# Optimization experiments

Hardware: AMD Instinct MI355X
Metric: run time of the kernel (lower is better)

## Reference

```python
import jax, jax.numpy as jnp
import numpy as np

N = 50_000      # nodes
E = 500_000     # directed edges
EMB = 500       # emb_dim (fixed by module)
OUT = 119       # decoder out_dim (num atom types)
L = 5           # encoder num_layer
BN_EPS = 1e-5


def setup_inputs() -> dict:
    key = jax.random.key(0)
    ks = jax.random.split(key, 20)
    d = {}
    # int graph inputs
    atom_type = jax.random.randint(ks[0], (N,), 0, 119)
    chirality = jax.random.randint(ks[1], (N,), 0, 3)
    d["x"] = jnp.stack([atom_type, chirality], axis=1)
    d["edge_index"] = jax.random.randint(ks[2], (2, E), 0, N)
    bond_type = jax.random.randint(ks[3], (E,), 0, 4)  # real bonds (4 = self-loop token)
    bond_dir = jax.random.randint(ks[4], (E,), 0, 3)
    d["edge_attr"] = jnp.stack([bond_type, bond_dir], axis=1)
    d["masked_atom_mask"] = jax.random.bernoulli(ks[5], 0.25, (N,))
    # float params
    f = lambda k, s: (jax.random.normal(k, s) * 0.02).astype(jnp.float32)
    d["atom_emb1"] = f(ks[6], (120, EMB))
    d["atom_emb2"] = f(ks[7], (3, EMB))
    d["enc_eemb1"] = f(ks[8], (L, 6, EMB))
    d["enc_eemb2"] = f(ks[9], (L, 3, EMB))
    d["enc_W1"] = f(ks[10], (L, EMB, 2 * EMB))
    d["enc_b1"] = jnp.zeros((L, 2 * EMB), jnp.float32)
    d["enc_W2"] = f(ks[11], (L, 2 * EMB, EMB))
    d["enc_b2"] = jnp.zeros((L, EMB), jnp.float32)
    d["bn_gamma"] = jnp.ones((L, EMB), jnp.float32)
    d["bn_beta"] = jnp.zeros((L, EMB), jnp.float32)
    d["bn_mean"] = jnp.zeros((L, EMB), jnp.float32)
    d["bn_var"] = jnp.ones((L, EMB), jnp.float32)
    d["prelu_a"] = jnp.float32(0.25)
    d["n2d_W"] = f(ks[12], (EMB, EMB))  # Linear(500,500,bias=False)
    d["dec_eemb1"] = f(ks[13], (6, EMB))
    d["dec_eemb2"] = f(ks[14], (3, EMB))
    d["dec_W1"] = f(ks[15], (EMB, 2 * EMB))
    d["dec_b1"] = jnp.zeros((2 * EMB,), jnp.float32)
    d["dec_W2"] = f(ks[16], (2 * EMB, OUT))
    d["dec_b2"] = jnp.zeros((OUT,), jnp.float32)
    return d


def _gin(h, src, dst, eemb, W1, b1, W2, b2):
    # message = x_j + edge_emb ; aggr='add' ; update = MLP
    msg = h[src] + eemb                                   # [E+N, EMB]
    agg = jax.ops.segment_sum(msg, dst, num_segments=h.shape[0])
    return jax.nn.relu(agg @ W1 + b1) @ W2 + b2


def _forward(x, edge_index, edge_attr, masked_atom_mask,
             atom_emb1, atom_emb2, enc_eemb1, enc_eemb2, enc_W1, enc_b1,
             enc_W2, enc_b2, bn_gamma, bn_beta, bn_mean, bn_var,
             prelu_a, n2d_W, dec_eemb1, dec_eemb2, dec_W1, dec_b1, dec_W2, dec_b2):
    n = x.shape[0]
    loops = jnp.arange(n)
    src = jnp.concatenate([edge_index[0], loops])         # add self loops
    dst = jnp.concatenate([edge_index[1], loops])
    ea0 = jnp.concatenate([edge_attr[:, 0], jnp.full((n,), 4, edge_attr.dtype)])
    ea1 = jnp.concatenate([edge_attr[:, 1], jnp.zeros((n,), edge_attr.dtype)])

    # GNN encoder
    h = atom_emb1[x[:, 0]] + atom_emb2[x[:, 1]]           # [N, EMB]
    for l in range(L):
        eemb = enc_eemb1[l][ea0] + enc_eemb2[l][ea1]
        h = _gin(h, src, dst, eemb, enc_W1[l], enc_b1[l], enc_W2[l], enc_b2[l])
        # BatchNorm1d in eval mode (running stats)
        h = (h - bn_mean[l]) * jax.lax.rsqrt(bn_var[l] + BN_EPS) * bn_gamma[l] + bn_beta[l]
        if l < L - 1:
            h = jax.nn.relu(h)
        # drop_ratio=0 -> no dropout

    # encoder_to_decoder: PReLU -> Linear(bias=False)
    h = jnp.where(h >= 0, h, prelu_a * h) @ n2d_W
    # zero out masked atoms
    h = jnp.where(masked_atom_mask[:, None], jnp.float32(0), h)

    # GINConv decoder -> [N, 119]
    eemb = dec_eemb1[ea0] + dec_eemb2[ea1]
    return _gin(h, src, dst, eemb, dec_W1, dec_b1, dec_W2, dec_b2)


def reference(x, edge_index, edge_attr, masked_atom_mask,
              atom_emb1, atom_emb2, enc_eemb1, enc_eemb2, enc_W1, enc_b1,
              enc_W2, enc_b2, bn_gamma, bn_beta, bn_mean, bn_var,
              prelu_a, n2d_W, dec_eemb1, dec_eemb2, dec_W1, dec_b1, dec_W2, dec_b2):
    return _forward(x, edge_index, edge_attr, masked_atom_mask,
                    atom_emb1, atom_emb2, enc_eemb1, enc_eemb2, enc_W1, enc_b1,
                    enc_W2, enc_b2, bn_gamma, bn_beta, bn_mean, bn_var,
                    prelu_a, n2d_W, dec_eemb1, dec_eemb2, dec_W1, dec_b1,
                    dec_W2, dec_b2)
```

## Files before the change

### kernel.cpp

```cpp
#include <hip/hip_runtime.h>
#include <stdint.h>

typedef unsigned short u16;
typedef __bf16 bf16x8 __attribute__((ext_vector_type(8)));
typedef float f32x4 __attribute__((ext_vector_type(4)));

enum { EPI_TMP = 0, EPI_BN = 1, EPI_N2D = 2, EPI_OUT = 3, EPI_BNPRELU = 4 };

__device__ __forceinline__ u16 f2bf(float x) {
  unsigned int u = __float_as_uint(x);
  u += 0x7FFFu + ((u >> 16) & 1u);
  return (u16)(u >> 16);
}
__device__ __forceinline__ float bf2f(u16 b) {
  return __uint_as_float(((unsigned int)b) << 16);
}
__device__ __forceinline__ float bflo(unsigned int u) { return __uint_as_float(u << 16); }
__device__ __forceinline__ float bfhi(unsigned int u) { return __uint_as_float(u & 0xFFFF0000u); }
__device__ __forceinline__ ushort4 pack4(float a, float b, float c, float d) {
  return make_ushort4(f2bf(a), f2bf(b), f2bf(c), f2bf(d));
}

struct F4 { float x, y, z, w; };
__device__ __forceinline__ F4 ld4(const float* p) {
  float4 v = *(const float4*)p;
  return {v.x, v.y, v.z, v.w};
}

typedef const void __attribute__((address_space(1))) as1cv;
typedef void __attribute__((address_space(3))) as3v;
__device__ __forceinline__ void gld16(const void* g, void* l) {
  __builtin_amdgcn_global_load_lds((as1cv*)g, (as3v*)l, 16, 0, 0);
}


__global__ void k_detect(const unsigned int* __restrict__ m, int nwords, int* __restrict__ flag) {
  int viol = 0;
  for (int i = blockIdx.x * blockDim.x + threadIdx.x; i < nwords; i += gridDim.x * blockDim.x) {
    unsigned int u = m[i];
    if (u > 1u) viol |= 1;
    if (u != 0u && u != 0x3F800000u) viol |= 2;
  }
  if (viol) atomicOr(flag, viol);
}

__global__ void k_norm(const void* __restrict__ raw, const int* __restrict__ flag,
                       unsigned char* __restrict__ mout, int N) {
  int f = *flag;
  for (int v = blockIdx.x * blockDim.x + threadIdx.x; v < N; v += gridDim.x * blockDim.x) {
    unsigned char b;
    if ((f & 1) == 0)       b = (unsigned char)(((const int*)raw)[v] != 0);
    else if ((f & 2) == 0)  b = (unsigned char)(((const float*)raw)[v] != 0.0f);
    else                    b = (unsigned char)(((const unsigned char*)raw)[v] != 0);
    mout[v] = b;
  }
}

__global__ void k_count(const int* __restrict__ ei, int E, int* __restrict__ deg) {
  for (int e = blockIdx.x * blockDim.x + threadIdx.x; e < E; e += gridDim.x * blockDim.x)
    atomicAdd(&deg[ei[E + e]], 1);
}

__global__ __launch_bounds__(1024)
void k_scanA(const int* __restrict__ deg, int* __restrict__ out,
             int* __restrict__ bsum, int n) {
  __shared__ int lws[17];
  const int tid = threadIdx.x, lane = tid & 63, wv = tid >> 6;
  const int i = blockIdx.x * 1024 + tid;
  const int v = (i < n) ? deg[i] : 0;
  int x = v;
#pragma unroll
  for (int d = 1; d < 64; d <<= 1) {
    int y = __shfl_up(x, d, 64);
    if (lane >= d) x += y;
  }
  if (lane == 63) lws[wv] = x;
  __syncthreads();
  if (tid == 0) {
    int run = 0;
#pragma unroll
    for (int k = 0; k < 16; ++k) { int t = lws[k]; lws[k] = run; run += t; }
    lws[16] = run;
  }
  __syncthreads();
  if (i < n) out[i] = x - v + lws[wv];
  if (tid == 0) bsum[blockIdx.x] = lws[16];
}

__global__ void k_scanB(int* __restrict__ bsum, int* __restrict__ offN, int nc) {
  const int t = threadIdx.x;
  const int v = (t < nc) ? bsum[t] : 0;
  int x = v;
#pragma unroll
  for (int d = 1; d < 64; d <<= 1) {
    int y = __shfl_up(x, d, 64);
    if (t >= d) x += y;
  }
  if (t < nc) bsum[t] = x - v;
  if (t == nc - 1) *offN = x;
}

__global__ void k_scanC(int* __restrict__ off_, const int* __restrict__ bsum, int n) {
  int i = blockIdx.x * blockDim.x + threadIdx.x;
  if (i < n) off_[i] += bsum[i >> 10];
}

__global__ void k_fill(const int* __restrict__ ei, const int* __restrict__ ea, int E,
                       int* __restrict__ cur, int* __restrict__ elist) {
  for (int e = blockIdx.x * blockDim.x + threadIdx.x; e < E; e += gridDim.x * blockDim.x) {
    int s = ei[e];
    int d = ei[E + e];
    int a0 = ea[2 * e], a1 = ea[2 * e + 1];
    int pos = atomicAdd(&cur[d], 1);
    elist[pos] = s | (a0 << 20) | (a1 << 23);
  }
}

__global__ void k_counts(const int* __restrict__ off_, const int* __restrict__ elist,
                         unsigned char* __restrict__ cnts, int N) {
  int v = blockIdx.x * blockDim.x + threadIdx.x;
  if (v >= N) return;
  int c0=0,c1=0,c2=0,c3=0,c4=0,c5=0,d0=0,d1=0,d2=0;
  const int e1 = off_[v + 1];
  for (int e = off_[v]; e < e1; ++e) {
    int p = elist[e];
    int a = (p >> 20) & 7, b = (p >> 23) & 3;
    c0 += (a==0); c1 += (a==1); c2 += (a==2);
    c3 += (a==3); c4 += (a==4); c5 += (a==5);
    d0 += (b==0); d1 += (b==1); d2 += (b==2);
  }
  unsigned char* cp = cnts + v * 12;
  cp[0]=(unsigned char)c0; cp[1]=(unsigned char)c1; cp[2]=(unsigned char)c2;
  cp[3]=(unsigned char)c3; cp[4]=(unsigned char)c4; cp[5]=(unsigned char)c5;
  cp[6]=(unsigned char)d0; cp[7]=(unsigned char)d1; cp[8]=(unsigned char)d2;
}

__global__ void k_tab(const float* __restrict__ ee1, const float* __restrict__ ee2,
                      const float* __restrict__ de1, const float* __restrict__ de2,
                      float* __restrict__ tab) {
  int idx = blockIdx.x * blockDim.x + threadIdx.x;
  if (idx >= 54 * 512) return;
  int col = idx & 511, row = (idx >> 9) % 9, l = idx / (9 * 512);
  float v = 0.f;
  if (col < 500) {
    if (l < 5) v = (row < 6) ? ee1[((size_t)l * 6 + row) * 500 + col]
                             : ee2[((size_t)l * 3 + (row - 6)) * 500 + col];
    else       v = (row < 6) ? de1[(size_t)row * 500 + col]
                             : de2[(size_t)(row - 6) * 500 + col];
  }
  tab[idx] = v;
}

__global__ void k_conv_w(const float* __restrict__ src, u16* __restrict__ dst,
                         int K, int Nsrc, int Kpad, int Npad, int L) {
  size_t total = (size_t)L * Npad * Kpad;
  for (size_t idx = blockIdx.x * (size_t)blockDim.x + threadIdx.x; idx < total;
       idx += (size_t)gridDim.x * blockDim.x) {
    int k = (int)(idx % (size_t)Kpad);
    size_t r = idx / (size_t)Kpad;
    int n = (int)(r % (size_t)Npad);
    int l = (int)(r / (size_t)Npad);
    float v = 0.0f;
    if (k < K && n < Nsrc) v = src[((size_t)l * K + k) * Nsrc + n];
    dst[idx] = f2bf(v);
  }
}

__global__ void k_init_h(const int* __restrict__ x, const float* __restrict__ e1,
                         const float* __restrict__ e2, u16* __restrict__ h, int nReal) {
  int total = nReal * 128;
  for (int i = blockIdx.x * blockDim.x + threadIdx.x; i < total; i += gridDim.x * blockDim.x) {
    int v = i >> 7, q = i & 127, j = q << 2;
    u16* hp = h + ((size_t)v << 9) + j;
    if (j < 500) {
      int a = x[2 * v], c = x[2 * v + 1];
      F4 va = ld4(e1 + (size_t)a * 500 + j);
      F4 vc = ld4(e2 + (size_t)c * 500 + j);
      *(ushort4*)hp = pack4(va.x + vc.x, va.y + vc.y, va.z + vc.z, va.w + vc.w);
    } else {
      *(ushort4*)hp = make_ushort4(0, 0, 0, 0);
    }
  }
}

__device__ __forceinline__ void add8(float* s, uint4 u) {
  s[0] += bflo(u.x); s[1] += bfhi(u.x);
  s[2] += bflo(u.y); s[3] += bfhi(u.y);
  s[4] += bflo(u.z); s[5] += bfhi(u.z);
  s[6] += bflo(u.w); s[7] += bfhi(u.w);
}

__global__ __launch_bounds__(256)
void k_aggregate(const u16* __restrict__ h, const int* __restrict__ off_,
                 const int* __restrict__ elist, const unsigned char* __restrict__ cnts,
                 const float* __restrict__ tab, u16* __restrict__ agg, int nReal) {
  const int lane = threadIdx.x & 63, wv = threadIdx.x >> 6;
  const int v = (blockIdx.x << 2) | wv;
  if (v >= nReal) return;
  const int j = lane << 3;
  float s[8];
  {
    uint4 u = *(const uint4*)(h + ((size_t)v << 9) + j);
    s[0] = bflo(u.x); s[1] = bfhi(u.x); s[2] = bflo(u.y); s[3] = bfhi(u.y);
    s[4] = bflo(u.z); s[5] = bfhi(u.z); s[6] = bflo(u.w); s[7] = bfhi(u.w);
  }
  const int eE = off_[v + 1];
  int e = off_[v];
  for (; e + 4 <= eE; e += 4) {
    uint4 u0 = *(const uint4*)(h + ((size_t)(elist[e]     & 0xFFFFF) << 9) + j);
    uint4 u1 = *(const uint4*)(h + ((size_t)(elist[e + 1] & 0xFFFFF) << 9) + j);
    uint4 u2 = *(const uint4*)(h + ((size_t)(elist[e + 2] & 0xFFFFF) << 9) + j);
    uint4 u3 = *(const uint4*)(h + ((size_t)(elist[e + 3] & 0xFFFFF) << 9) + j);
    add8(s, u0); add8(s, u1); add8(s, u2); add8(s, u3);
  }
  for (; e < eE; ++e) {
    uint4 u = *(const uint4*)(h + ((size_t)(elist[e] & 0xFFFFF) << 9) + j);
    add8(s, u);
  }
  const unsigned char* cp = cnts + v * 12;
  constexpr float ex[9] = {0.f,0.f,0.f,0.f,1.f,0.f, 1.f,0.f,0.f};
#pragma unroll
  for (int k = 0; k < 9; ++k) {
    const float ck = (float)cp[k] + ex[k];
    F4 t0 = ld4(tab + (k << 9) + j);
    F4 t1 = ld4(tab + (k << 9) + j + 4);
    s[0] += ck * t0.x; s[1] += ck * t0.y; s[2] += ck * t0.z; s[3] += ck * t0.w;
    s[4] += ck * t1.x; s[5] += ck * t1.y; s[6] += ck * t1.z; s[7] += ck * t1.w;
  }
  auto pk = [](float a, float b) {
    return (unsigned int)f2bf(a) | ((unsigned int)f2bf(b) << 16);
  };
  uint4 o = {pk(s[0], s[1]), pk(s[2], s[3]), pk(s[4], s[5]), pk(s[6], s[7])};
  *(uint4*)(agg + ((size_t)v << 9) + j) = o;
}

struct EpiParams {
  const float* bias;
  const float* mean; const float* var; const float* gamma; const float* beta;
  const unsigned char* mask;
  const float* pa;
  float* outF;
  u16* outH;
  int ldOut, nReal, mReal, relu;
};

#define EPI_STRIDE 136

template<int EPI>
__global__ __launch_bounds__(256, 3)
void k_gemm(const u16* __restrict__ A, const u16* __restrict__ B,
            int ldA, int Kpad, int Ntiles, int NWG, EpiParams P) {
  __shared__ __align__(16) u16 smem[128 * EPI_STRIDE];

  const int tid = threadIdx.x;
  const int w = tid >> 6, lane = tid & 63;
  const int q = NWG >> 3, r = NWG & 7;
  const int xcd = blockIdx.x & 7, ii = blockIdx.x >> 3;
  const int wg = (xcd < r ? xcd * (q + 1) : r * (q + 1) + (xcd - r) * q) + ii;
  const int mt = wg / Ntiles, nt = wg % Ntiles;
  const int wm = w >> 1, wn = w & 1;

  f32x4 acc[4][4] = {};
  const size_t arow = (size_t)mt * 128, brow = (size_t)nt * 128;
  const int Ksteps = Kpad >> 6;

  for (int ks = 0; ks < Ksteps; ++ks) {
    const int kb = ks << 6;
#pragma unroll
    for (int it = 0; it < 4; ++it) {
      const int idx = (it << 8) | tid;
      const int row = idx >> 3, s = idx & 7;
      const int col = kb + ((s ^ (row & 7)) << 3);
      u16* dst = smem + (((it << 8) | (w << 6)) << 3);
      gld16(A + (arow + row) * (size_t)ldA + col, dst);
      gld16(B + (brow + row) * (size_t)Kpad + col, dst + 8192);
    }
    asm volatile("s_waitcnt vmcnt(0)" ::: "memory");
    __syncthreads();

#pragma unroll
    for (int kk = 0; kk < 2; ++kk) {
      const int ko8 = (kk << 2) | (lane >> 4);
      const int sw = (ko8 ^ (lane & 7)) << 3;
      bf16x8 af[4], bfr[4];
#pragma unroll
      for (int m = 0; m < 4; ++m)
        af[m] = *(const bf16x8*)(smem + ((((wm << 6) | (m << 4) | (lane & 15))) << 6) + sw);
#pragma unroll
      for (int n = 0; n < 4; ++n)
        bfr[n] = *(const bf16x8*)(smem + 8192 + ((((wn << 6) | (n << 4) | (lane & 15))) << 6) + sw);
#pragma unroll
      for (int m = 0; m < 4; ++m)
#pragma unroll
        for (int n = 0; n < 4; ++n)
          acc[m][n] = __builtin_amdgcn_mfma_f32_16x16x32_bf16(af[m], bfr[n], acc[m][n], 0, 0, 0);
    }
    __syncthreads();
  }

  const int rb0 = mt * 128, cb0 = nt * 128;
  const int rloc = (wm << 6) | ((lane >> 4) << 2);
  const int cloc = (wn << 6) | (lane & 15);

  if constexpr (EPI != EPI_OUT) {
    float alpha = 0.f;
    if constexpr (EPI == EPI_BNPRELU) alpha = *P.pa;
#pragma unroll
    for (int n = 0; n < 4; ++n) {
      const int col = cloc + (n << 4);
      const int colg = cb0 + col;
      const bool cok = colg < P.nReal;
      float bias = 0.f, bnS = 0.f, bnB = 0.f;
      if constexpr (EPI == EPI_TMP) {
        if (cok) bias = P.bias[colg];
      }
      if constexpr (EPI == EPI_BN || EPI == EPI_BNPRELU) {
        if (cok) {
          bias = P.bias[colg];
          bnS = rsqrtf(P.var[colg] + 1e-5f) * P.gamma[colg];
          bnB = P.beta[colg] - P.mean[colg] * bnS;
        }
      }
#pragma unroll
      for (int m = 0; m < 4; ++m) {
#pragma unroll
        for (int rr = 0; rr < 4; ++rr) {
          const int row = rloc + (m << 4) + rr;
          float z = acc[m][n][rr];
          if constexpr (EPI == EPI_TMP) {
            z = fmaxf(z + bias, 0.f);
          } else if constexpr (EPI == EPI_BN) {
            z = (z + bias) * bnS + bnB;
            if (P.relu) z = fmaxf(z, 0.f);
          } else if constexpr (EPI == EPI_BNPRELU) {
            z = (z + bias) * bnS + bnB;
            z = z >= 0.f ? z : alpha * z;
          } else {
            const int rowg = rb0 + row;
            if (rowg < P.mReal && P.mask[rowg]) z = 0.f;
          }
          smem[row * EPI_STRIDE + col] = f2bf(z);
        }
      }
    }
    __syncthreads();
#pragma unroll
    for (int it = 0; it < 8; ++it) {
      const int idx = (it << 8) | tid;
      const int row = idx >> 4, c8 = idx & 15;
      uint4 vv = *(const uint4*)(smem + row * EPI_STRIDE + (c8 << 3));
      *(uint4*)(P.outH + (size_t)(rb0 + row) * P.ldOut + cb0 + (c8 << 3)) = vv;
    }
  } else {
    float* sf = (float*)smem;
#pragma unroll
    for (int p = 0; p < 2; ++p) {
      __syncthreads();
      if (wm == p) {
#pragma unroll
        for (int n = 0; n < 4; ++n) {
          const int col = cloc + (n << 4);
          const float bias = (cb0 + col < P.nReal) ? P.bias[cb0 + col] : 0.f;
#pragma unroll
          for (int m = 0; m < 4; ++m)
#pragma unroll
            for (int rr = 0; rr < 4; ++rr) {
              const int lrow = ((lane >> 4) << 2) + (m << 4) + rr;
              sf[lrow * 132 + col] = acc[m][n][rr] + bias;
            }
        }
      }
      __syncthreads();
      const size_t flat0 = (size_t)(rb0 + (p << 6)) * 119;
      const size_t flatEnd = (size_t)P.mReal * 119;
#pragma unroll 2
      for (int it = 0; it < 30; ++it) {
        const int fidx = it * 256 + tid;
        if (fidx < 64 * 119) {
          const int row = fidx / 119;
          const int col = fidx - row * 119;
          const size_t g = flat0 + fidx;
          if (g < flatEnd) P.outF[g] = sf[row * 132 + col];
        }
      }
    }
  }
}

__global__ void k_fail(float* out, int n, float val) {
  for (int i = blockIdx.x * blockDim.x + threadIdx.x; i < n; i += gridDim.x * blockDim.x)
    out[i] = (i == 0) ? val : 0.f;
}

static inline size_t alup(size_t x) { return (x + 255) & ~(size_t)255; }

extern "C" void kernel_launch(void* const* d_in, const int* in_sizes, int n_in,
                              void* d_out, int out_size, void* d_ws, size_t ws_size,
                              hipStream_t stream) {
  (void)n_in;
  const int N = in_sizes[0] / 2;
  const int E = in_sizes[1] / 2;
  const int Mpad = (N + 127) / 128 * 128;
  const int MT = Mpad / 128;

  size_t off = 0;
  auto plan = [&](size_t b) -> size_t { size_t p = off; off += alup(b); return p; };
  const size_t o_h    = plan((size_t)Mpad * 512 * 2);
  const size_t o_agg  = plan((size_t)Mpad * 512 * 2);
  const size_t o_tmp  = plan((size_t)Mpad * 1024 * 2);
  const size_t o_w1   = plan(5ull * 1024 * 512 * 2);
  const size_t o_w2   = plan(5ull * 512 * 1024 * 2);
  const size_t o_nd   = plan(512ull * 512 * 2);
  const size_t o_d1   = plan(1024ull * 512 * 2);
  const size_t o_d2   = plan(128ull * 1024 * 2);
  const size_t o_tab  = plan(54ull * 512 * 4);
  const size_t o_offv = plan((size_t)(N + 1) * 4);
  const size_t o_cur  = plan((size_t)N * 4);
  const size_t o_el   = plan((size_t)E * 4);
  const size_t o_mask = plan((size_t)N);
  const size_t o_cnt  = plan((size_t)N * 12);
  const size_t o_bsum = plan(1024);
  const size_t o_flag = plan(256);
  const size_t need = off;

  if (ws_size < need) {
    k_fail<<<1024, 256, 0, stream>>>((float*)d_out, out_size, -(float)(ws_size >> 20));
    return;
  }

  char* ws = (char*)d_ws;
  u16* h     = (u16*)(ws + o_h);
  u16* agg   = (u16*)(ws + o_agg);
  u16* tmp   = (u16*)(ws + o_tmp);
  u16* w1H   = (u16*)(ws + o_w1);
  u16* w2H   = (u16*)(ws + o_w2);
  u16* ndH   = (u16*)(ws + o_nd);
  u16* d1H   = (u16*)(ws + o_d1);
  u16* d2H   = (u16*)(ws + o_d2);
  float* tab = (float*)(ws + o_tab);
  int* offv  = (int*)(ws + o_offv);
  int* cur   = (int*)(ws + o_cur);
  int* elist = (int*)(ws + o_el);
  unsigned char* mask = (unsigned char*)(ws + o_mask);
  unsigned char* cnts = (unsigned char*)(ws + o_cnt);
  int* bsum  = (int*)(ws + o_bsum);
  int* flag  = (int*)(ws + o_flag);

  const int* x   = (const int*)d_in[0];
  const int* ei  = (const int*)d_in[1];
  const int* ea  = (const int*)d_in[2];
  const void* mraw = d_in[3];
  const float* ae1 = (const float*)d_in[4];
  const float* ae2 = (const float*)d_in[5];
  const float* ee1 = (const float*)d_in[6];
  const float* ee2 = (const float*)d_in[7];
  const float* W1  = (const float*)d_in[8];
  const float* b1  = (const float*)d_in[9];
  const float* W2  = (const float*)d_in[10];
  const float* b2  = (const float*)d_in[11];
  const float* gamma = (const float*)d_in[12];
  const float* beta  = (const float*)d_in[13];
  const float* mean  = (const float*)d_in[14];
  const float* var   = (const float*)d_in[15];
  const float* pa    = (const float*)d_in[16];
  const float* n2dW  = (const float*)d_in[17];
  const float* de1   = (const float*)d_in[18];
  const float* de2   = (const float*)d_in[19];
  const float* dW1   = (const float*)d_in[20];
  const float* db1   = (const float*)d_in[21];
  const float* dW2   = (const float*)d_in[22];
  const float* db2   = (const float*)d_in[23];

  hipMemsetAsync(flag, 0, 4, stream);
  hipMemsetAsync(cur, 0, (size_t)N * 4, stream);
  k_detect<<<256, 256, 0, stream>>>((const unsigned int*)mraw, N / 4, flag);
  k_norm<<<(N + 255) / 256, 256, 0, stream>>>(mraw, flag, mask, N);
  k_count<<<2048, 256, 0, stream>>>(ei, E, cur);
  const int nchunks = (N + 1023) / 1024;
  k_scanA<<<nchunks, 1024, 0, stream>>>(cur, offv, bsum, N);
  k_scanB<<<1, 64, 0, stream>>>(bsum, offv + N, nchunks);
  k_scanC<<<(N + 255) / 256, 256, 0, stream>>>(offv, bsum, N);
  hipMemcpyAsync(cur, offv, (size_t)N * 4, hipMemcpyDeviceToDevice, stream);
  k_fill<<<2048, 256, 0, stream>>>(ei, ea, E, cur, elist);
  k_counts<<<(N + 255) / 256, 256, 0, stream>>>(offv, elist, cnts, N);
  k_tab<<<(54 * 512 + 255) / 256, 256, 0, stream>>>(ee1, ee2, de1, de2, tab);

  k_conv_w<<<2048, 256, 0, stream>>>(W1, w1H, 500, 1000, 512, 1024, 5);
  k_conv_w<<<2048, 256, 0, stream>>>(W2, w2H, 1000, 500, 1024, 512, 5);
  k_conv_w<<<1024, 256, 0, stream>>>(n2dW, ndH, 500, 500, 512, 512, 1);
  k_conv_w<<<1024, 256, 0, stream>>>(dW1, d1H, 500, 1000, 512, 1024, 1);
  k_conv_w<<<1024, 256, 0, stream>>>(dW2, d2H, 1000, 119, 1024, 128, 1);
  k_init_h<<<4096, 256, 0, stream>>>(x, ae1, ae2, h, N);

  const int aggGrid = (N + 3) / 4;
  EpiParams P{};

  for (int l = 0; l < 5; ++l) {
    k_aggregate<<<aggGrid, 256, 0, stream>>>(h, offv, elist, cnts,
                                             tab + (size_t)l * 9 * 512, agg, N);
    P = EpiParams{};
    P.bias = b1 + (size_t)l * 1000;
    P.outH = tmp; P.ldOut = 1024; P.nReal = 1000; P.mReal = Mpad; P.relu = 1;
    k_gemm<EPI_TMP><<<MT * 8, 256, 0, stream>>>(
        agg, w1H + (size_t)l * 1024 * 512, 512, 512, 8, MT * 8, P);

    P = EpiParams{};
    P.bias = b2 + (size_t)l * 500;
    P.mean = mean + (size_t)l * 500; P.var = var + (size_t)l * 500;
    P.gamma = gamma + (size_t)l * 500; P.beta = beta + (size_t)l * 500;
    if (l < 4) {
      P.outH = h; P.ldOut = 512; P.nReal = 500; P.mReal = Mpad; P.relu = 1;
      k_gemm<EPI_BN><<<MT * 4, 256, 0, stream>>>(
          tmp, w2H + (size_t)l * 512 * 1024, 1024, 1024, 4, MT * 4, P);
    } else {
      P.pa = pa;
      P.outH = agg; P.ldOut = 512; P.nReal = 500; P.mReal = Mpad; P.relu = 0;
      k_gemm<EPI_BNPRELU><<<MT * 4, 256, 0, stream>>>(
          tmp, w2H + (size_t)l * 512 * 1024, 1024, 1024, 4, MT * 4, P);
    }
  }

  P = EpiParams{};
  P.outH = h; P.mask = mask; P.ldOut = 512; P.nReal = 500; P.mReal = N;
  k_gemm<EPI_N2D><<<MT * 4, 256, 0, stream>>>(agg, ndH, 512, 512, 4, MT * 4, P);

  k_aggregate<<<aggGrid, 256, 0, stream>>>(h, offv, elist, cnts,
                                           tab + (size_t)5 * 9 * 512, agg, N);
  P = EpiParams{};
  P.bias = db1; P.outH = tmp; P.ldOut = 1024; P.nReal = 1000; P.mReal = Mpad; P.relu = 1;
  k_gemm<EPI_TMP><<<MT * 8, 256, 0, stream>>>(agg, d1H, 512, 512, 8, MT * 8, P);

  P = EpiParams{};
  P.bias = db2; P.outF = (float*)d_out; P.ldOut = 119; P.nReal = 119; P.mReal = N;
  k_gemm<EPI_OUT><<<MT * 1, 256, 0, stream>>>(tmp, d2H, 1024, 1024, 1, MT, P);
}
```

Measured before the change: 1.377 ms.

## Shrink GEMM shared memory for higher occupancy and unroll aggregation by eight

The GEMM kernel's shared buffer drops from 128x136 to 16384 halfwords. The epilogue now writes and stores the output tile in two 64-row halves, each written by one wave-row group, and launch bounds ask for 4 workgroups per CU instead of 3. The aggregation kernel gains an 8-way unrolled neighbour gather to put more loads in flight. The risks are extra epilogue barriers and register pressure from the tighter launch bound. The fp32 output epilogue's stride of 128 without padding may also cause LDS bank conflicts.

```diff
diff --git a/kernel.cpp b/kernel.cpp
--- a/kernel.cpp
+++ b/kernel.cpp
@@ -206,6 +206,22 @@
   }
   const int eE = off_[v + 1];
   int e = off_[v];
+  for (; e + 8 <= eE; e += 8) {
+    const int p0 = elist[e]     & 0xFFFFF, p1 = elist[e + 1] & 0xFFFFF;
+    const int p2 = elist[e + 2] & 0xFFFFF, p3 = elist[e + 3] & 0xFFFFF;
+    const int p4 = elist[e + 4] & 0xFFFFF, p5 = elist[e + 5] & 0xFFFFF;
+    const int p6 = elist[e + 6] & 0xFFFFF, p7 = elist[e + 7] & 0xFFFFF;
+    uint4 u0 = *(const uint4*)(h + ((size_t)p0 << 9) + j);
+    uint4 u1 = *(const uint4*)(h + ((size_t)p1 << 9) + j);
+    uint4 u2 = *(const uint4*)(h + ((size_t)p2 << 9) + j);
+    uint4 u3 = *(const uint4*)(h + ((size_t)p3 << 9) + j);
+    uint4 u4 = *(const uint4*)(h + ((size_t)p4 << 9) + j);
+    uint4 u5 = *(const uint4*)(h + ((size_t)p5 << 9) + j);
+    uint4 u6 = *(const uint4*)(h + ((size_t)p6 << 9) + j);
+    uint4 u7 = *(const uint4*)(h + ((size_t)p7 << 9) + j);
+    add8(s, u0); add8(s, u1); add8(s, u2); add8(s, u3);
+    add8(s, u4); add8(s, u5); add8(s, u6); add8(s, u7);
+  }
   for (; e + 4 <= eE; e += 4) {
     uint4 u0 = *(const uint4*)(h + ((size_t)(elist[e]     & 0xFFFFF) << 9) + j);
     uint4 u1 = *(const uint4*)(h + ((size_t)(elist[e + 1] & 0xFFFFF) << 9) + j);
@@ -244,13 +260,11 @@
   int ldOut, nReal, mReal, relu;
 };
 
-#define EPI_STRIDE 136
-
 template<int EPI>
-__global__ __launch_bounds__(256, 3)
+__global__ __launch_bounds__(256, 4)
 void k_gemm(const u16* __restrict__ A, const u16* __restrict__ B,
             int ldA, int Kpad, int Ntiles, int NWG, EpiParams P) {
-  __shared__ __align__(16) u16 smem[128 * EPI_STRIDE];
+  __shared__ __align__(16) u16 smem[16384];
 
   const int tid = threadIdx.x;
   const int w = tid >> 6, lane = tid & 63;
@@ -299,60 +313,25 @@
   }
 
   const int rb0 = mt * 128, cb0 = nt * 128;
-  const int rloc = (wm << 6) | ((lane >> 4) << 2);
+  const int fq = lane >> 4;
   const int cloc = (wn << 6) | (lane & 15);
 
   if constexpr (EPI != EPI_OUT) {
     float alpha = 0.f;
     if constexpr (EPI == EPI_BNPRELU) alpha = *P.pa;
+    float bias4[4] = {}, bnS4[4] = {}, bnB4[4] = {};
 #pragma unroll
     for (int n = 0; n < 4; ++n) {
-      const int col = cloc + (n << 4);
-      const int colg = cb0 + col;
-      const bool cok = colg < P.nReal;
-      float bias = 0.f, bnS = 0.f, bnB = 0.f;
-      if constexpr (EPI == EPI_TMP) {
-        if (cok) bias = P.bias[colg];
-      }
-      if constexpr (EPI == EPI_BN || EPI == EPI_BNPRELU) {
-        if (cok) {
-          bias = P.bias[colg];
-          bnS = rsqrtf(P.var[colg] + 1e-5f) * P.gamma[colg];
-          bnB = P.beta[colg] - P.mean[colg] * bnS;
+      const int colg = cb0 + cloc + (n << 4);
+      if (colg < P.nReal) {
+        if constexpr (EPI == EPI_TMP) bias4[n] = P.bias[colg];
+        if constexpr (EPI == EPI_BN || EPI == EPI_BNPRELU) {
+          bias4[n] = P.bias[colg];
+          bnS4[n] = rsqrtf(P.var[colg] + 1e-5f) * P.gamma[colg];
+          bnB4[n] = P.beta[colg] - P.mean[colg] * bnS4[n];
         }
       }
-#pragma unroll
-      for (int m = 0; m < 4; ++m) {
-#pragma unroll
-        for (int rr = 0; rr < 4; ++rr) {
-          const int row = rloc + (m << 4) + rr;
-          float z = acc[m][n][rr];
-          if constexpr (EPI == EPI_TMP) {
-            z = fmaxf(z + bias, 0.f);
-          } else if constexpr (EPI == EPI_BN) {
-            z = (z + bias) * bnS + bnB;
-            if (P.relu) z = fmaxf(z, 0.f);
-          } else if constexpr (EPI == EPI_BNPRELU) {
-            z = (z + bias) * bnS + bnB;
-            z = z >= 0.f ? z : alpha * z;
-          } else {
-            const int rowg = rb0 + row;
-            if (rowg < P.mReal && P.mask[rowg]) z = 0.f;
-          }
-          smem[row * EPI_STRIDE + col] = f2bf(z);
-        }
-      }
-    }
-    __syncthreads();
-#pragma unroll
-    for (int it = 0; it < 8; ++it) {
-      const int idx = (it << 8) | tid;
-      const int row = idx >> 4, c8 = idx & 15;
-      uint4 vv = *(const uint4*)(smem + row * EPI_STRIDE + (c8 << 3));
-      *(uint4*)(P.outH + (size_t)(rb0 + row) * P.ldOut + cb0 + (c8 << 3)) = vv;
-    }
-  } else {
-    float* sf = (float*)smem;
+    }
 #pragma unroll
     for (int p = 0; p < 2; ++p) {
       __syncthreads();
@@ -360,13 +339,54 @@
 #pragma unroll
         for (int n = 0; n < 4; ++n) {
           const int col = cloc + (n << 4);
+#pragma unroll
+          for (int m = 0; m < 4; ++m) {
+#pragma unroll
+            for (int rr = 0; rr < 4; ++rr) {
+              const int lrow = (m << 4) + (fq << 2) + rr;
+              float z = acc[m][n][rr];
+              if constexpr (EPI == EPI_TMP) {
+                z = fmaxf(z + bias4[n], 0.f);
+              } else if constexpr (EPI == EPI_BN) {
+                z = (z + bias4[n]) * bnS4[n] + bnB4[n];
+                if (P.relu) z = fmaxf(z, 0.f);
+              } else if constexpr (EPI == EPI_BNPRELU) {
+                z = (z + bias4[n]) * bnS4[n] + bnB4[n];
+                z = z >= 0.f ? z : alpha * z;
+              } else {
+                const int rowg = rb0 + (p << 6) + lrow;
+                if (rowg < P.mReal && P.mask[rowg]) z = 0.f;
+              }
+              smem[lrow * 136 + col] = f2bf(z);
+            }
+          }
+        }
+      }
+      __syncthreads();
+#pragma unroll
+      for (int it = 0; it < 4; ++it) {
+        const int idx = (it << 8) | tid;
+        const int row = idx >> 4, c8 = idx & 15;
+        uint4 vv = *(const uint4*)(smem + row * 136 + (c8 << 3));
+        *(uint4*)(P.outH + (size_t)(rb0 + (p << 6) + row) * P.ldOut + cb0 + (c8 << 3)) = vv;
+      }
+    }
+  } else {
+    float* sf = (float*)smem;
+#pragma unroll
+    for (int p = 0; p < 2; ++p) {
+      __syncthreads();
+      if (wm == p) {
+#pragma unroll
+        for (int n = 0; n < 4; ++n) {
+          const int col = cloc + (n << 4);
           const float bias = (cb0 + col < P.nReal) ? P.bias[cb0 + col] : 0.f;
 #pragma unroll
           for (int m = 0; m < 4; ++m)
 #pragma unroll
             for (int rr = 0; rr < 4; ++rr) {
-              const int lrow = ((lane >> 4) << 2) + (m << 4) + rr;
-              sf[lrow * 132 + col] = acc[m][n][rr] + bias;
+              const int lrow = (fq << 2) + (m << 4) + rr;
+              sf[lrow * 128 + col] = acc[m][n][rr] + bias;
             }
         }
       }
@@ -380,7 +400,7 @@
           const int row = fidx / 119;
           const int col = fidx - row * 119;
           const size_t g = flat0 + fidx;
-          if (g < flatEnd) P.outF[g] = sf[row * 132 + col];
+          if (g < flatEnd) P.outF[g] = sf[row * 128 + col];
         }
       }
     }
```

New measurement: 1.400 ms. Within noise of the previous version (+1.6%).
